# Performance work log

Measured on AMD Instinct MI355X. Metric: run time of the kernel, lower is better.

Reference implementation:

```python
import jax, jax.numpy as jnp
import numpy as np

B, C, T, D = 256, 2, 25, 4096
H = 512          # LSTM units (num_features)
H1 = 128         # fc1 hidden
NC = 2           # num_classes
LEAKY_ALPHA = 0.2  # tf.nn.leaky_relu default


def setup_inputs() -> dict:
    key = jax.random.key(0)
    ks = jax.random.split(key, 8)
    return {
        "x": jax.random.normal(ks[0], (B, C, T, D), dtype=jnp.float32),
        "kernel": jax.random.normal(ks[1], (D, 4 * H), dtype=jnp.float32) * 0.02,
        "rec_kernel": jax.random.normal(ks[2], (H, 4 * H), dtype=jnp.float32) * 0.02,
        "bias": jax.random.normal(ks[3], (4 * H,), dtype=jnp.float32) * 0.02,
        "w1": jax.random.normal(ks[4], (H, H1), dtype=jnp.float32) * 0.05,
        "b1": jax.random.normal(ks[5], (H1,), dtype=jnp.float32) * 0.05,
        "w2": jax.random.normal(ks[6], (H1, NC), dtype=jnp.float32) * 0.05,
        "b2": jax.random.normal(ks[7], (NC,), dtype=jnp.float32) * 0.05,
    }


def _lstm(xc, kernel, rec_kernel, bias):
    # xc: [B, T, D]; Keras gate order i, f, c(g), o
    h = xc.shape[0], rec_kernel.shape[0]
    zx = jnp.einsum('btd,dg->btg', xc, kernel) + bias      # [B, T, 4H]
    zx_t = jnp.swapaxes(zx, 0, 1)                           # [T, B, 4H]
    nH = rec_kernel.shape[0]
    h0 = jnp.zeros((xc.shape[0], nH), dtype=xc.dtype)
    c0 = jnp.zeros((xc.shape[0], nH), dtype=xc.dtype)

    def step(carry, z_in):
        h, c = carry
        z = z_in + h @ rec_kernel                           # [B, 4H]
        i, f, g, o = jnp.split(z, 4, axis=-1)
        i = jax.nn.sigmoid(i)
        f = jax.nn.sigmoid(f)
        g = jnp.tanh(g)
        o = jax.nn.sigmoid(o)
        c = f * c + i * g
        h = o * jnp.tanh(c)
        return (h, c), None

    (hT, _), _ = jax.lax.scan(step, (h0, c0), zx_t)
    return hT                                               # [B, H]


def reference(x, kernel, rec_kernel, bias, w1, b1, w2, b2):
    xc = x[:, 0]                                            # rgb channel (ix=0)
    h = _lstm(xc, kernel, rec_kernel, bias)
    y = jax.nn.leaky_relu(h @ w1 + b1, negative_slope=LEAKY_ALPHA)
    # dropout inactive at inference (training=False)
    return jax.nn.softmax(y @ w2 + b2, axis=-1)             # [B, NC]
```

## Files before the change

kernel.cpp:

```cpp
#include <hip/hip_runtime.h>


typedef __bf16 bf16x8 __attribute__((ext_vector_type(8)));
typedef float  f32x4  __attribute__((ext_vector_type(4)));

#define MFMA16(a, b, c) __builtin_amdgcn_mfma_f32_16x16x32_bf16((a), (b), (c), 0, 0, 0)

__device__ __forceinline__ float sigmf(float x) {
  return 1.0f / (1.0f + __expf(-x));
}
__device__ __forceinline__ float tanhf_(float x) {
  float a = fabsf(x);
  float e = __expf(-2.0f * a);
  float r = (1.0f - e) / (1.0f + e);
  return copysignf(r, x);
}

__device__ __forceinline__ void async16(__bf16* lds, const __bf16* g) {
  __builtin_amdgcn_global_load_lds(
      (const __attribute__((address_space(1))) unsigned int*)g,
      (__attribute__((address_space(3))) unsigned int*)lds, 16, 0, 0);
}

__global__ __launch_bounds__(256) void conv_xb(const float* __restrict__ x,
                                               __bf16* __restrict__ xb) {
  long o = ((long)blockIdx.x * 256 + threadIdx.x) * 8;
  int m = (int)(o >> 12);
  int k = (int)(o & 4095);
  int b = m / 25, t = m - b * 25;
  const float* src = x + (long)b * 204800 + (long)t * 4096 + k;
  f32x4 v0 = *(const f32x4*)src;
  f32x4 v1 = *(const f32x4*)(src + 4);
  bf16x8 r;
  r[0] = (__bf16)v0[0]; r[1] = (__bf16)v0[1];
  r[2] = (__bf16)v0[2]; r[3] = (__bf16)v0[3];
  r[4] = (__bf16)v1[0]; r[5] = (__bf16)v1[1];
  r[6] = (__bf16)v1[2]; r[7] = (__bf16)v1[3];
  *(bf16x8*)(xb + o) = r;
}

__global__ __launch_bounds__(256) void conv_wkT(const float* __restrict__ wk,
                                                __bf16* __restrict__ wkT) {
  __shared__ float tile[64][65];
  const int k0 = blockIdx.y * 64;
  const int n0 = blockIdx.x * 64;
  const int tx = threadIdx.x & 63;
  const int ty = threadIdx.x >> 6;
#pragma unroll
  for (int p = 0; p < 16; ++p) {
    int kr = ty + p * 4;
    tile[kr][tx] = wk[(long)(k0 + kr) * 2048 + n0 + tx];
  }
  __syncthreads();
#pragma unroll
  for (int p = 0; p < 16; ++p) {
    int nr = ty + p * 4;
    wkT[(long)(n0 + nr) * 4096 + k0 + tx] = (__bf16)tile[tx][nr];
  }
}

__global__ __launch_bounds__(256) void conv_recF(const float* __restrict__ rec,
                                                 __bf16* __restrict__ recF) {
  int o = blockIdx.x * 256 + threadIdx.x;
  int i  = o & 7;
  int l  = (o >> 3) & 63;
  int ks = (o >> 9) & 15;
  int jt = (o >> 13) & 31;
  int g  = o >> 18;
  int k = ks * 32 + ((l >> 4) << 3) + i;
  int n = g * 512 + jt * 16 + (l & 15);
  recF[o] = (__bf16)rec[(long)k * 2048 + n];
}

__global__ __launch_bounds__(256) void gemm_bf16(const __bf16* __restrict__ A,
                                                 const __bf16* __restrict__ Bt,
                                                 const float* __restrict__ bias,
                                                 float* __restrict__ zx) {
  __shared__ __bf16 As[128 * 64];
  __shared__ __bf16 Bs[128 * 64];
  const int tid  = threadIdx.x;
  const int wid  = tid >> 6;
  const int lane = tid & 63;
  const int m0 = blockIdx.y * 128;
  const int n0 = blockIdx.x * 128;

  const int srow  = (wid << 3) + (lane >> 3);
  const int skoff = (lane & 7) << 3;

  const int wr   = (wid >> 1) << 6;
  const int wc   = (wid & 1) << 6;
  const int lrow = lane & 15;
  const int lk8  = (lane >> 4) << 3;

  f32x4 acc[4][4];
#pragma unroll
  for (int i = 0; i < 4; ++i)
#pragma unroll
    for (int j = 0; j < 4; ++j) {
      f32x4 z = {0.f, 0.f, 0.f, 0.f};
      acc[i][j] = z;
    }

  const __bf16* Ag = A  + (long)(m0 + srow) * 4096 + skoff;
  const __bf16* Bg = Bt + (long)(n0 + srow) * 4096 + skoff;
  __bf16* Al = &As[(wid << 3) * 64];
  __bf16* Bl = &Bs[(wid << 3) * 64];

  for (int k0 = 0; k0 < 4096; k0 += 64) {
    __syncthreads();
#pragma unroll
    for (int q = 0; q < 4; ++q) {
      async16(Al + q * (32 * 64), Ag + (long)(q * 32) * 4096 + k0);
      async16(Bl + q * (32 * 64), Bg + (long)(q * 32) * 4096 + k0);
    }
    __syncthreads();
#pragma unroll
    for (int kk = 0; kk < 2; ++kk) {
      bf16x8 af[4], bv[4];
#pragma unroll
      for (int fr = 0; fr < 4; ++fr)
        af[fr] = *(const bf16x8*)&As[(wr + fr * 16 + lrow) * 64 + (kk << 5) + lk8];
#pragma unroll
      for (int fc = 0; fc < 4; ++fc)
        bv[fc] = *(const bf16x8*)&Bs[(wc + fc * 16 + lrow) * 64 + (kk << 5) + lk8];
#pragma unroll
      for (int fr = 0; fr < 4; ++fr)
#pragma unroll
        for (int fc = 0; fc < 4; ++fc)
          acc[fr][fc] = MFMA16(af[fr], bv[fc], acc[fr][fc]);
    }
  }

  const int mlow = (lane >> 4) << 2;
#pragma unroll
  for (int fc = 0; fc < 4; ++fc) {
    int n = n0 + wc + fc * 16 + lrow;
    float bvs = bias[n];
#pragma unroll
    for (int fr = 0; fr < 4; ++fr) {
      int mb = m0 + wr + fr * 16 + mlow;
#pragma unroll
      for (int r = 0; r < 4; ++r)
        zx[(long)(mb + r) * 2048 + n] = acc[fr][fc][r] + bvs;
    }
  }
}

__global__ __launch_bounds__(256) void lstm_step2(const float* __restrict__ zx,
                                                  const __bf16* __restrict__ recF,
                                                  const __bf16* __restrict__ hFin,
                                                  __bf16* __restrict__ hFout,
                                                  float* __restrict__ cbuf,
                                                  __bf16* __restrict__ hplain,
                                                  int t, int last) {
  const int tid  = threadIdx.x;
  const int wid  = tid >> 6;
  const int lane = tid & 63;
  const int jt = blockIdx.x;
  const int rt = (blockIdx.y << 2) + wid;

  f32x4 acc[4];
#pragma unroll
  for (int g = 0; g < 4; ++g) {
    f32x4 z = {0.f, 0.f, 0.f, 0.f};
    acc[g] = z;
  }

#pragma unroll 4
  for (int ks = 0; ks < 16; ++ks) {
    bf16x8 a = *(const bf16x8*)(hFin + ((((rt << 4) + ks) << 6) + lane) * 8);
#pragma unroll
    for (int g = 0; g < 4; ++g) {
      bf16x8 b = *(const bf16x8*)(recF +
          ((((((g << 5) + jt) << 4) + ks) << 6) + lane) * 8);
      acc[g] = MFMA16(a, b, acc[g]);
    }
  }

  const int j    = (jt << 4) + (lane & 15);
  const int mlow = (lane >> 4) << 2;
  const int ks2  = j >> 5;
  const int lhi  = ((j >> 3) & 3) << 4;
  const int i2   = j & 7;

#pragma unroll
  for (int r = 0; r < 4; ++r) {
    int brow = (rt << 4) + mlow + r;
    long zb = ((long)(brow * 25 + t)) << 11;
    float zi = acc[0][r] + zx[zb + j];
    float zf = acc[1][r] + zx[zb + 512 + j];
    float zg = acc[2][r] + zx[zb + 1024 + j];
    float zo = acc[3][r] + zx[zb + 1536 + j];
    float ig = sigmf(zi);
    float fg = sigmf(zf);
    float gg = tanhf_(zg);
    float og = sigmf(zo);
    int ci = (brow << 9) + j;
    float cn = fg * cbuf[ci] + ig * gg;
    cbuf[ci] = cn;
    float hv = og * tanhf_(cn);
    hFout[((((rt << 4) + ks2) << 6) + (lhi | (brow & 15))) * 8 + i2] = (__bf16)hv;
    if (last) hplain[ci] = (__bf16)hv;
  }
}

__global__ __launch_bounds__(128) void head_kernel(const __bf16* __restrict__ h,
                                                   const float* __restrict__ w1,
                                                   const float* __restrict__ b1,
                                                   const float* __restrict__ w2,
                                                   const float* __restrict__ b2,
                                                   float* __restrict__ out) {
  const int b = blockIdx.x;
  const int j = threadIdx.x;
  float acc = b1[j];
#pragma unroll 8
  for (int k = 0; k < 512; ++k)
    acc += (float)h[b * 512 + k] * w1[k * 128 + j];
  float y = acc > 0.f ? acc : 0.2f * acc;

  __shared__ float s0[128], s1[128];
  s0[j] = y * w2[j * 2 + 0];
  s1[j] = y * w2[j * 2 + 1];
  __syncthreads();
#pragma unroll
  for (int s = 64; s > 0; s >>= 1) {
    if (j < s) { s0[j] += s0[j + s]; s1[j] += s1[j + s]; }
    __syncthreads();
  }
  if (j == 0) {
    float l0 = s0[0] + b2[0];
    float l1 = s1[0] + b2[1];
    float m  = fmaxf(l0, l1);
    float e0 = __expf(l0 - m);
    float e1 = __expf(l1 - m);
    float inv = 1.0f / (e0 + e1);
    out[b * 2 + 0] = e0 * inv;
    out[b * 2 + 1] = e1 * inv;
  }
}

extern "C" void kernel_launch(void* const* d_in, const int* in_sizes, int n_in,
                              void* d_out, int out_size, void* d_ws, size_t ws_size,
                              hipStream_t stream) {
  const float* x    = (const float*)d_in[0];
  const float* wk   = (const float*)d_in[1];
  const float* rec  = (const float*)d_in[2];
  const float* bias = (const float*)d_in[3];
  const float* w1   = (const float*)d_in[4];
  const float* b1   = (const float*)d_in[5];
  const float* w2   = (const float*)d_in[6];
  const float* b2   = (const float*)d_in[7];
  float* out = (float*)d_out;

  char* w = (char*)d_ws;
  float*  zx     = (float*)(w + 0);
  __bf16* xb     = (__bf16*)(w + 52428800);
  __bf16* wkT    = (__bf16*)(w + 104857600);
  __bf16* recF   = (__bf16*)(w + 121634816);
  __bf16* hA     = (__bf16*)(w + 123731968);
  __bf16* hB     = (__bf16*)(w + 123994112);
  float*  cbuf   = (float*)(w + 124256256);
  __bf16* hplain = (__bf16*)(w + 124780544);

  hipMemsetAsync(hA, 0, 262144, stream);
  hipMemsetAsync(cbuf, 0, 524288, stream);

  conv_xb  <<<12800, 256, 0, stream>>>(x, xb);
  conv_wkT <<<dim3(32, 64), 256, 0, stream>>>(wk, wkT);
  conv_recF<<<4096, 256, 0, stream>>>(rec, recF);

  gemm_bf16<<<dim3(16, 50), 256, 0, stream>>>(xb, wkT, bias, zx);

  for (int t = 0; t < 25; ++t) {
    const __bf16* hin = (t & 1) ? hB : hA;
    __bf16* hout      = (t & 1) ? hA : hB;
    lstm_step2<<<dim3(32, 4), 256, 0, stream>>>(zx, recF, hin, hout, cbuf,
                                                hplain, t, (t == 24) ? 1 : 0);
  }
  head_kernel<<<256, 128, 0, stream>>>(hplain, w1, b1, w2, b2, out);
}
```

Measured before the change: 755.8 us.

## Fuse LSTM time steps into one persistent kernel with grid barrier

Replaces the 25 per-timestep LSTM launches with a single persistent kernel of 128 blocks. Each block keeps its recurrent-weight slice in LDS and the cell state in registers, and uses an atomic grid-wide barrier between steps. The GEMM now writes zx in time-major order and remaps its block index for L2 locality. The recurrent-weight conversion uses an LDS-tiled transpose with vector stores. This removes launch overhead and repeated global loads of weights and cell state, but depends on all 128 blocks being co-resident and adds barrier spin latency on every step.

```diff
diff --git a/kernel.cpp b/kernel.cpp
--- a/kernel.cpp
+++ b/kernel.cpp
@@ -59,30 +59,46 @@
   }
 }
 
-__global__ __launch_bounds__(256) void conv_recF(const float* __restrict__ rec,
-                                                 __bf16* __restrict__ recF) {
-  int o = blockIdx.x * 256 + threadIdx.x;
-  int i  = o & 7;
-  int l  = (o >> 3) & 63;
-  int ks = (o >> 9) & 15;
-  int jt = (o >> 13) & 31;
-  int g  = o >> 18;
-  int k = ks * 32 + ((l >> 4) << 3) + i;
-  int n = g * 512 + jt * 16 + (l & 15);
-  recF[o] = (__bf16)rec[(long)k * 2048 + n];
+__global__ __launch_bounds__(256) void conv_recF2(const float* __restrict__ rec,
+                                                  __bf16* __restrict__ recF) {
+  __shared__ float tile[512][17];
+  const int tid = threadIdx.x;
+  const int g  = blockIdx.x >> 5;
+  const int jt = blockIdx.x & 31;
+#pragma unroll 4
+  for (int p = 0; p < 32; ++p) {
+    int k = (p << 4) + (tid >> 4);
+    tile[k][tid & 15] = rec[(long)k * 2048 + (g << 9) + (jt << 4) + (tid & 15)];
+  }
+  __syncthreads();
+  const int l = tid & 63;
+  const int w = tid >> 6;
+  long obase = ((long)((g * 32 + jt) * 16)) * 512;
+#pragma unroll
+  for (int q = 0; q < 4; ++q) {
+    int ks = (w << 2) + q;
+    bf16x8 v;
+#pragma unroll
+    for (int i = 0; i < 8; ++i)
+      v[i] = (__bf16)tile[(ks << 5) + ((l >> 4) << 3) + i][l & 15];
+    *(bf16x8*)(recF + obase + (long)ks * 512 + l * 8) = v;
+  }
 }
 
 __global__ __launch_bounds__(256) void gemm_bf16(const __bf16* __restrict__ A,
                                                  const __bf16* __restrict__ Bt,
                                                  const float* __restrict__ bias,
-                                                 float* __restrict__ zx) {
+                                                 float* __restrict__ zxr) {
   __shared__ __bf16 As[128 * 64];
   __shared__ __bf16 Bs[128 * 64];
   const int tid  = threadIdx.x;
   const int wid  = tid >> 6;
   const int lane = tid & 63;
-  const int m0 = blockIdx.y * 128;
-  const int n0 = blockIdx.x * 128;
+
+  const int bid = blockIdx.x;
+  const int swz = (bid & 7) * 100 + (bid >> 3);
+  const int m0 = (swz >> 4) << 7;
+  const int n0 = (swz & 15) << 7;
 
   const int srow  = (wid << 3) + (lane >> 3);
   const int skoff = (lane & 7) << 3;
@@ -96,9 +112,9 @@
 #pragma unroll
   for (int i = 0; i < 4; ++i)
 #pragma unroll
-    for (int j = 0; j < 4; ++j) {
+    for (int jj = 0; jj < 4; ++jj) {
       f32x4 z = {0.f, 0.f, 0.f, 0.f};
-      acc[i][j] = z;
+      acc[i][jj] = z;
     }
 
   const __bf16* Ag = A  + (long)(m0 + srow) * 4096 + skoff;
@@ -140,41 +156,39 @@
     for (int fr = 0; fr < 4; ++fr) {
       int mb = m0 + wr + fr * 16 + mlow;
 #pragma unroll
-      for (int r = 0; r < 4; ++r)
-        zx[(long)(mb + r) * 2048 + n] = acc[fr][fc][r] + bvs;
-    }
-  }
-}
-
-__global__ __launch_bounds__(256) void lstm_step2(const float* __restrict__ zx,
-                                                  const __bf16* __restrict__ recF,
-                                                  const __bf16* __restrict__ hFin,
-                                                  __bf16* __restrict__ hFout,
-                                                  float* __restrict__ cbuf,
-                                                  __bf16* __restrict__ hplain,
-                                                  int t, int last) {
+      for (int r = 0; r < 4; ++r) {
+        int m = mb + r;
+        int b = m / 25;
+        int tt = m - b * 25;
+        zxr[((long)((tt << 8) + b) << 11) + n] = acc[fr][fc][r] + bvs;
+      }
+    }
+  }
+}
+
+__global__ __launch_bounds__(256) void lstm_persist(const float* __restrict__ zxr,
+                                                    const __bf16* __restrict__ recF,
+                                                    __bf16* __restrict__ hA,
+                                                    __bf16* __restrict__ hB,
+                                                    __bf16* __restrict__ hplain,
+                                                    int* bar) {
+  __shared__ __bf16 recS[32768];
   const int tid  = threadIdx.x;
   const int wid  = tid >> 6;
   const int lane = tid & 63;
-  const int jt = blockIdx.x;
-  const int rt = (blockIdx.y << 2) + wid;
-
-  f32x4 acc[4];
-#pragma unroll
-  for (int g = 0; g < 4; ++g) {
-    f32x4 z = {0.f, 0.f, 0.f, 0.f};
-    acc[g] = z;
-  }
-
-#pragma unroll 4
-  for (int ks = 0; ks < 16; ++ks) {
-    bf16x8 a = *(const bf16x8*)(hFin + ((((rt << 4) + ks) << 6) + lane) * 8);
-#pragma unroll
-    for (int g = 0; g < 4; ++g) {
-      bf16x8 b = *(const bf16x8*)(recF +
-          ((((((g << 5) + jt) << 4) + ks) << 6) + lane) * 8);
-      acc[g] = MFMA16(a, b, acc[g]);
-    }
+  const int bid  = blockIdx.x;
+  const int jt   = bid & 31;
+  const int rtg  = bid >> 5;
+  const int rt   = (rtg << 2) + wid;
+
+  {
+    const __bf16* src = recF + (long)(jt << 4) * 512;
+#pragma unroll
+    for (int g = 0; g < 4; ++g)
+#pragma unroll
+      for (int q = 0; q < 4; ++q)
+        *(bf16x8*)(recS + g * 8192 + q * 2048 + tid * 8) =
+            *(const bf16x8*)(src + (long)g * 262144 + q * 2048 + tid * 8);
   }
 
   const int j    = (jt << 4) + (lane & 15);
@@ -182,25 +196,81 @@
   const int ks2  = j >> 5;
   const int lhi  = ((j >> 3) & 3) << 4;
   const int i2   = j & 7;
-
+  float c[4];
+  int brow[4];
 #pragma unroll
   for (int r = 0; r < 4; ++r) {
-    int brow = (rt << 4) + mlow + r;
-    long zb = ((long)(brow * 25 + t)) << 11;
-    float zi = acc[0][r] + zx[zb + j];
-    float zf = acc[1][r] + zx[zb + 512 + j];
-    float zg = acc[2][r] + zx[zb + 1024 + j];
-    float zo = acc[3][r] + zx[zb + 1536 + j];
-    float ig = sigmf(zi);
-    float fg = sigmf(zf);
-    float gg = tanhf_(zg);
-    float og = sigmf(zo);
-    int ci = (brow << 9) + j;
-    float cn = fg * cbuf[ci] + ig * gg;
-    cbuf[ci] = cn;
-    float hv = og * tanhf_(cn);
-    hFout[((((rt << 4) + ks2) << 6) + (lhi | (brow & 15))) * 8 + i2] = (__bf16)hv;
-    if (last) hplain[ci] = (__bf16)hv;
+    c[r] = 0.f;
+    brow[r] = (rt << 4) + mlow + r;
+  }
+  __syncthreads();
+
+  float zv[4][4];
+#pragma unroll
+  for (int g = 0; g < 4; ++g)
+#pragma unroll
+    for (int r = 0; r < 4; ++r)
+      zv[g][r] = zxr[((long)brow[r] << 11) + (g << 9) + j];
+
+  const __bf16* hin = hA;
+  __bf16* hout = hA;
+
+  for (int t = 0; t < 25; ++t) {
+    if (t > 0) {
+      f32x4 acc[4];
+#pragma unroll
+      for (int g = 0; g < 4; ++g) {
+        f32x4 z = {0.f, 0.f, 0.f, 0.f};
+        acc[g] = z;
+      }
+#pragma unroll 4
+      for (int ks = 0; ks < 16; ++ks) {
+        bf16x8 a = *(const bf16x8*)(hin + ((((rt << 4) + ks) << 6) + lane) * 8);
+#pragma unroll
+        for (int g = 0; g < 4; ++g) {
+          bf16x8 b = *(const bf16x8*)(recS + ((((g << 4) + ks) << 6) + lane) * 8);
+          acc[g] = MFMA16(a, b, acc[g]);
+        }
+      }
+#pragma unroll
+      for (int g = 0; g < 4; ++g)
+#pragma unroll
+        for (int r = 0; r < 4; ++r)
+          zv[g][r] += acc[g][r];
+    }
+
+#pragma unroll
+    for (int r = 0; r < 4; ++r) {
+      float ig = sigmf(zv[0][r]);
+      float fg = sigmf(zv[1][r]);
+      float gg = tanhf_(zv[2][r]);
+      float og = sigmf(zv[3][r]);
+      float cn = fg * c[r] + ig * gg;
+      c[r] = cn;
+      float hv = og * tanhf_(cn);
+      hout[((((rt << 4) + ks2) << 6) + (lhi | (brow[r] & 15))) * 8 + i2] = (__bf16)hv;
+      if (t == 24) hplain[(brow[r] << 9) + j] = (__bf16)hv;
+    }
+
+    if (t < 24) {
+#pragma unroll
+      for (int g = 0; g < 4; ++g)
+#pragma unroll
+        for (int r = 0; r < 4; ++r)
+          zv[g][r] = zxr[((long)(((t + 1) << 8) + brow[r]) << 11) + (g << 9) + j];
+
+      __syncthreads();
+      if (tid == 0) {
+        __hip_atomic_fetch_add(bar, 1, __ATOMIC_RELEASE, __HIP_MEMORY_SCOPE_AGENT);
+        const int target = 128 * (t + 1);
+        while (__hip_atomic_load(bar, __ATOMIC_ACQUIRE, __HIP_MEMORY_SCOPE_AGENT) < target)
+          __builtin_amdgcn_s_sleep(2);
+      }
+      __syncthreads();
+    }
+
+    hin  = hout;
+    hout = (t & 1) ? hA : hB;
   }
 }
 
@@ -253,29 +323,24 @@
   float* out = (float*)d_out;
 
   char* w = (char*)d_ws;
-  float*  zx     = (float*)(w + 0);
+  float*  zxr    = (float*)(w + 0);
   __bf16* xb     = (__bf16*)(w + 52428800);
   __bf16* wkT    = (__bf16*)(w + 104857600);
   __bf16* recF   = (__bf16*)(w + 121634816);
   __bf16* hA     = (__bf16*)(w + 123731968);
   __bf16* hB     = (__bf16*)(w + 123994112);
-  float*  cbuf   = (float*)(w + 124256256);
-  __bf16* hplain = (__bf16*)(w + 124780544);
-
-  hipMemsetAsync(hA, 0, 262144, stream);
-  hipMemsetAsync(cbuf, 0, 524288, stream);
-
-  conv_xb  <<<12800, 256, 0, stream>>>(x, xb);
-  conv_wkT <<<dim3(32, 64), 256, 0, stream>>>(wk, wkT);
-  conv_recF<<<4096, 256, 0, stream>>>(rec, recF);
-
-  gemm_bf16<<<dim3(16, 50), 256, 0, stream>>>(xb, wkT, bias, zx);
-
-  for (int t = 0; t < 25; ++t) {
-    const __bf16* hin = (t & 1) ? hB : hA;
-    __bf16* hout      = (t & 1) ? hA : hB;
-    lstm_step2<<<dim3(32, 4), 256, 0, stream>>>(zx, recF, hin, hout, cbuf,
-                                                hplain, t, (t == 24) ? 1 : 0);
-  }
+  __bf16* hplain = (__bf16*)(w + 124256256);
+  int*    bar    = (int*)(w + 124518400);
+
+  hipMemsetAsync(bar, 0, 256, stream);
+
+  conv_xb   <<<12800, 256, 0, stream>>>(x, xb);
+  conv_wkT  <<<dim3(32, 64), 256, 0, stream>>>(wk, wkT);
+  conv_recF2<<<128, 256, 0, stream>>>(rec, recF);
+
+  gemm_bf16<<<800, 256, 0, stream>>>(xb, wkT, bias, zxr);
+
+  lstm_persist<<<128, 256, 0, stream>>>(zxr, recF, hA, hB, hplain, bar);
+
   head_kernel<<<256, 128, 0, stream>>>(hplain, w1, b1, w2, b2, out);
 }
```

New measurement: 781.2 us. 1.03x slower.
